# Kernel optimization log

Measured on AMD Instinct MI355X. Metric: run time of the kernel, lower is better.

## Reference

```python
import jax, jax.numpy as jnp
import numpy as np

N, E, F, H, C, K = 100000, 1600000, 512, 256, 64, 10
EPS = 1e-5  # BatchNorm1d default eps


def setup_inputs() -> dict:
    key = jax.random.key(0)
    ks = jax.random.split(key, 8)
    x = jax.random.normal(ks[0], (N, F), jnp.float32)
    # edge list with no self-loops (gcn_norm adds the self-loops itself)
    src = jax.random.randint(ks[1], (E,), 0, N)
    off = jax.random.randint(ks[2], (E,), 1, N)
    dst = (src + off) % N
    edge_index = jnp.stack([src, dst])
    s = lambda k, sh: jax.random.normal(k, sh, jnp.float32) * 0.02
    W0 = s(ks[3], (F, H)); b0 = jnp.zeros((H,), jnp.float32)
    g0 = jnp.ones((H,), jnp.float32); be0 = jnp.zeros((H,), jnp.float32)
    W1 = s(ks[4], (H, H)); b1 = jnp.zeros((H,), jnp.float32)
    g1 = jnp.ones((H,), jnp.float32); be1 = jnp.zeros((H,), jnp.float32)
    W2 = s(ks[5], (H, C)); b2 = jnp.zeros((C,), jnp.float32)
    proj_w = s(ks[6], (C, 1)); proj_b = jnp.zeros((1,), jnp.float32)
    return dict(x=x, W0=W0, b0=b0, g0=g0, be0=be0, W1=W1, b1=b1, g1=g1,
                be1=be1, W2=W2, b2=b2, proj_w=proj_w, proj_b=proj_b,
                edge_index=edge_index)


def _batchnorm(h, gamma, beta):
    # training-mode BN over the node (batch) axis, biased variance like torch
    mu = h.mean(0)
    var = h.var(0)
    return gamma * (h - mu) * jax.lax.rsqrt(var + EPS) + beta


def _prop(x, edge_index, proj_w, proj_b):
    n, c = x.shape
    loop = jnp.arange(n, dtype=edge_index.dtype)
    row = jnp.concatenate([edge_index[0], loop])  # message sources (x_j)
    col = jnp.concatenate([edge_index[1], loop])  # aggregation targets
    w = jnp.ones(row.shape, x.dtype)
    deg = jax.ops.segment_sum(w, col, num_segments=n)
    dis = jnp.where(deg > 0, jax.lax.rsqrt(jnp.maximum(deg, 1.0)) * (deg > 0), 0.0)
    dis = jnp.where(deg > 0, deg ** -0.5, 0.0)
    norm = dis[row] * dis[col]  # symmetric GCN normalization per edge

    def hop(xk, _):
        msgs = norm[:, None] * xk[row]               # gather + scale  [E+N, C]
        xk = jax.ops.segment_sum(msgs, col, num_segments=n)  # scatter-add
        return xk, xk

    _, hops = jax.lax.scan(hop, x, None, length=K)   # [K, N, C]
    pps = jnp.concatenate([x[None], hops], axis=0).transpose(1, 0, 2)  # [N, K+1, C]
    score = jax.nn.sigmoid(pps @ proj_w + proj_b)[..., 0]  # [N, K+1]
    return jnp.einsum('nk,nkc->nc', score, pps)      # [N, C]


def reference(x, W0, b0, g0, be0, W1, b1, g1, be1, W2, b2, proj_w, proj_b,
              edge_index):
    h = jax.nn.relu(_batchnorm(x @ W0 + b0, g0, be0))   # dropout is identity (eval)
    h = jax.nn.relu(_batchnorm(h @ W1 + b1, g1, be1))
    h = h @ W2 + b2                                     # [N, C] logits
    out = _prop(h, edge_index, proj_w, proj_b)
    return jax.nn.log_softmax(out, axis=1)
```

## Files before the change

### kernel.cpp

```cpp
#include <hip/hip_runtime.h>
#include <hip/hip_bf16.h>
#include <math.h>

#define NN 100000
#define FF 512
#define HH 256
#define CC 64
#define KHOPS 10
#define BN_EPS 1e-5f
#define NPART 8
#define DRANGE ((NN + NPART - 1) / NPART)

typedef __bf16 bf16x8 __attribute__((ext_vector_type(8)));
typedef float f32x4 __attribute__((ext_vector_type(4)));
typedef unsigned short ushort8v __attribute__((ext_vector_type(8)));

__device__ __forceinline__ unsigned short f2bf(float f) {
    __bf16 b = (__bf16)f;
    return __builtin_bit_cast(unsigned short, b);
}
__device__ __forceinline__ float bf2f(unsigned short h) {
    unsigned u = ((unsigned)h) << 16;
    return __builtin_bit_cast(float, u);
}
__device__ __forceinline__ float lo16(unsigned u) { return bf2f((unsigned short)(u & 0xFFFF)); }
__device__ __forceinline__ float hi16(unsigned u) { return bf2f((unsigned short)(u >> 16)); }
__device__ __forceinline__ unsigned pk(float a, float b) {
    return ((unsigned)f2bf(b) << 16) | (unsigned)f2bf(a);
}

typedef __attribute__((address_space(1))) const void g_void;
typedef __attribute__((address_space(3))) void l_void;
__device__ __forceinline__ void gl2lds16(const void* g, void* l) {
    __builtin_amdgcn_global_load_lds((g_void*)g, (l_void*)l, 16, 0, 0);
}

template <int N>
__device__ __forceinline__ void waitcnt_vm() {
    if constexpr (N == 0) asm volatile("s_waitcnt vmcnt(0)" ::: "memory");
    else if constexpr (N == 1) asm volatile("s_waitcnt vmcnt(1)" ::: "memory");
    else if constexpr (N == 2) asm volatile("s_waitcnt vmcnt(2)" ::: "memory");
    else if constexpr (N == 3) asm volatile("s_waitcnt vmcnt(3)" ::: "memory");
    else if constexpr (N == 4) asm volatile("s_waitcnt vmcnt(4)" ::: "memory");
    else if constexpr (N == 5) asm volatile("s_waitcnt vmcnt(5)" ::: "memory");
    else if constexpr (N == 6) asm volatile("s_waitcnt vmcnt(6)" ::: "memory");
    else asm volatile("s_waitcnt vmcnt(8)" ::: "memory");
}

__global__ void k_zero(float* p, int n) {
    int i = blockIdx.x * blockDim.x + threadIdx.x;
    if (i < n) p[i] = 0.f;
}

__global__ void k_deg_init(int* deg, int n) {
    int i = blockIdx.x * blockDim.x + threadIdx.x;
    if (i < n) deg[i] = 1;
}

__global__ __launch_bounds__(256) void k_deg_part(const int* __restrict__ dst, int e,
                                                  int* __restrict__ deg) {
    __shared__ int hist[DRANGE];
    int part = blockIdx.x & 7;
    int lo = part * DRANGE;
    int range = min(DRANGE, NN - lo);
    for (int i = threadIdx.x; i < range; i += blockDim.x) hist[i] = 0;
    __syncthreads();
    int nsub = gridDim.x >> 3, sub = blockIdx.x >> 3;
    for (int i = sub * blockDim.x + threadIdx.x; i < e; i += nsub * blockDim.x) {
        int d = dst[i] - lo;
        if ((unsigned)d < (unsigned)range) atomicAdd(&hist[d], 1);
    }
    __syncthreads();
    for (int i = threadIdx.x; i < range; i += blockDim.x) {
        int v = hist[i];
        if (v) atomicAdd(&deg[lo + i], v);
    }
}

__global__ void k_dis(const int* __restrict__ deg, float* dis, int n) {
    int i = blockIdx.x * blockDim.x + threadIdx.x;
    if (i < n) dis[i] = rsqrtf((float)deg[i]);
}

#define SCAN_B 1024
#define SCAN_NB ((NN + SCAN_B - 1) / SCAN_B)

__global__ void k_scan1(const int* __restrict__ deg, int* __restrict__ part, int n) {
    __shared__ int ls[SCAN_B];
    int i = blockIdx.x * SCAN_B + threadIdx.x;
    ls[threadIdx.x] = (i < n) ? deg[i] - 1 : 0;
    __syncthreads();
    for (int d = SCAN_B / 2; d > 0; d >>= 1) {
        if (threadIdx.x < d) ls[threadIdx.x] += ls[threadIdx.x + d];
        __syncthreads();
    }
    if (threadIdx.x == 0) part[blockIdx.x] = ls[0];
}

__global__ void k_scan2(int* part, int* offs_last, int nb) {
    if (threadIdx.x == 0) {
        int run = 0;
        for (int b = 0; b < nb; b++) { int v = part[b]; part[b] = run; run += v; }
        offs_last[0] = run;
    }
}

__global__ void k_scan3(const int* __restrict__ deg, const int* __restrict__ part,
                        int* __restrict__ offs, int* __restrict__ cur, int n) {
    __shared__ int ls[SCAN_B];
    int i = blockIdx.x * SCAN_B + threadIdx.x;
    int v = (i < n) ? deg[i] - 1 : 0;
    ls[threadIdx.x] = v;
    __syncthreads();
    for (int d = 1; d < SCAN_B; d <<= 1) {
        int t = (threadIdx.x >= d) ? ls[threadIdx.x - d] : 0;
        __syncthreads();
        ls[threadIdx.x] += t;
        __syncthreads();
    }
    if (i < n) {
        int ex = part[blockIdx.x] + ls[threadIdx.x] - v;
        offs[i] = ex;
        cur[i] = ex;
    }
}

__global__ __launch_bounds__(256) void k_fill_part(
    const int* __restrict__ src, const int* __restrict__ dst, int e,
    int* __restrict__ cursor, int* __restrict__ csrc) {
    int part = blockIdx.x & 7;
    int lo = part * DRANGE;
    int range = min(DRANGE, NN - lo);
    int nsub = gridDim.x >> 3, sub = blockIdx.x >> 3;
    for (int i = sub * blockDim.x + threadIdx.x; i < e; i += nsub * blockDim.x) {
        int d = dst[i];
        int dl = d - lo;
        if ((unsigned)dl < (unsigned)range) {
            int p = atomicAdd(&cursor[d], 1);
            csrc[p] = src[i];
        }
    }
}

__global__ void k_wt(const float* __restrict__ W, unsigned short* __restrict__ Wt,
                     int K, int N) {
    int i = blockIdx.x * blockDim.x + threadIdx.x;
    if (i < K * N) {
        int n = i / K;
        int k = i - n * K;
        Wt[i] = f2bf(W[(size_t)k * N + n]);
    }
}

template <int AF32, int BN_, int STATS, int NW, int FUSEBN, int ZSCALE>
__global__ __launch_bounds__(NW * 64) void k_gemm_mfma(
    const void* __restrict__ Av, const unsigned short* __restrict__ Bt,
    const float* __restrict__ bias, unsigned short* __restrict__ Cb,
    const float* __restrict__ bnscale, const float* __restrict__ bnshift,
    const float* __restrict__ disp,
    float* __restrict__ sum, float* __restrict__ sumsq,
    int M, int K, int Nd) {
    constexpr int NT = NW * 64;
    constexpr int WC = (NW == 8) ? 4 : 2;
    constexpr int PWN = BN_ / WC;
    constexpr int NREP = PWN / 16;
    constexpr int ACH = AF32 ? 8 : 4;
    constexpr int AOPS = 128 * ACH / NT;
    constexpr int BOPS = BN_ * 4 / NT;
    constexpr int S = AOPS + BOPS;
    constexpr int ABUF = AF32 ? 16384 : 8192;
    __shared__ __align__(16) unsigned char Asb[2][ABUF];
    __shared__ __align__(16) unsigned char Bsb[2][BN_ * 64];
    const int tid = threadIdx.x;
    const int lane = tid & 63;
    const int wid = tid >> 6;
    const int wrow = wid / WC, wcol = wid % WC;
    const int row_base = blockIdx.y * 128;
    const int col_base = blockIdx.x * BN_;
    const unsigned char* Abase = (const unsigned char*)Av;
    const size_t arowb = (size_t)K * (AF32 ? 4 : 2);

    f32x4 acc[4][NREP];
#pragma unroll
    for (int m = 0; m < 4; m++)
#pragma unroll
        for (int n = 0; n < NREP; n++)
#pragma unroll
            for (int j = 0; j < 4; j++) acc[m][n][j] = 0.f;

    auto stage = [&](int kt, int buf) {
#pragma unroll
        for (int i = 0; i < AOPS; ++i) {
            int e = i * NT + tid;
            int r = e / ACH;
            int c = e % ACH;
            int cs = AF32 ? (c ^ (r & 7)) : (c ^ ((r >> 1) & 3));
            int grow = row_base + r;
            if (grow > M - 1) grow = M - 1;
            const void* g = Abase + (size_t)grow * arowb + (size_t)kt * (AF32 ? 4 : 2) + (cs << 4);
            gl2lds16(g, Asb[buf] + e * 16);
        }
#pragma unroll
        for (int i = 0; i < BOPS; ++i) {
            int e = i * NT + tid;
            int r = e >> 2, c = e & 3;
            int cs = c ^ ((r >> 1) & 3);
            const void* g = (const unsigned char*)Bt + (size_t)(col_base + r) * (K * 2) +
                            (size_t)kt * 2 + (cs << 4);
            gl2lds16(g, Bsb[buf] + e * 16);
        }
    };

    const int nt = K / 32;
    stage(0, 0);
    if (nt > 1) stage(32, 1);

    for (int t = 0; t < nt; ++t) {
        if (t + 1 < nt) waitcnt_vm<S>();
        else            waitcnt_vm<0>();
        __builtin_amdgcn_s_barrier();
        const int cur = t & 1;

        f32x4 sc0{}, sc1{}, sh0{}, sh1{};
        if (FUSEBN) {
            int kc = t * 32 + (lane >> 4) * 8;
            sc0 = *(const f32x4*)(bnscale + kc);
            sc1 = *(const f32x4*)(bnscale + kc + 4);
            sh0 = *(const f32x4*)(bnshift + kc);
            sh1 = *(const f32x4*)(bnshift + kc + 4);
        }

        bf16x8 af[4], bfr[NREP];
#pragma unroll
        for (int m = 0; m < 4; ++m) {
            int r = wrow * 64 + m * 16 + (lane & 15);
            if (AF32) {
                int x7 = r & 7;
                int q2 = (lane >> 4) * 2;
                f32x4 f0 = *(const f32x4*)(Asb[cur] + r * 128 + ((q2 ^ x7) << 4));
                f32x4 f1 = *(const f32x4*)(Asb[cur] + r * 128 + (((q2 + 1) ^ x7) << 4));
                bf16x8 a;
                a[0] = (__bf16)f0[0]; a[1] = (__bf16)f0[1]; a[2] = (__bf16)f0[2]; a[3] = (__bf16)f0[3];
                a[4] = (__bf16)f1[0]; a[5] = (__bf16)f1[1]; a[6] = (__bf16)f1[2]; a[7] = (__bf16)f1[3];
                af[m] = a;
            } else {
                int cs = (lane >> 4) ^ ((r >> 1) & 3);
                bf16x8 a = *(const bf16x8*)(Asb[cur] + r * 64 + (cs << 4));
                if (FUSEBN) {
#pragma unroll
                    for (int j = 0; j < 4; ++j) {
                        a[j]     = (__bf16)fmaxf((float)a[j]     * sc0[j] + sh0[j], 0.f);
                        a[j + 4] = (__bf16)fmaxf((float)a[j + 4] * sc1[j] + sh1[j], 0.f);
                    }
                }
                af[m] = a;
            }
        }
#pragma unroll
        for (int n = 0; n < NREP; ++n) {
            int r = wcol * PWN + n * 16 + (lane & 15);
            int cs = (lane >> 4) ^ ((r >> 1) & 3);
            bfr[n] = *(const bf16x8*)(Bsb[cur] + r * 64 + (cs << 4));
        }
#pragma unroll
        for (int m = 0; m < 4; ++m)
#pragma unroll
            for (int n = 0; n < NREP; ++n)
                acc[m][n] = __builtin_amdgcn_mfma_f32_16x16x32_bf16(af[m], bfr[n], acc[m][n], 0, 0, 0);

        __builtin_amdgcn_s_barrier();
        if (t + 2 < nt) stage((t + 2) * 32, cur);
    }

    const int lc = lane & 15;
    const int lr = (lane >> 4) * 4;
#pragma unroll
    for (int m = 0; m < 4; ++m) {
        int gr0 = row_base + wrow * 64 + m * 16 + lr;
#pragma unroll
        for (int n = 0; n < NREP; ++n) {
            int gc = col_base + wcol * PWN + n * 16 + lc;
            float bb = bias[gc];
#pragma unroll
            for (int j = 0; j < 4; ++j) {
                int gr = gr0 + j;
                if (gr < M) {
                    float v = acc[m][n][j] + bb;
                    if (ZSCALE) v *= disp[gr];
                    Cb[(size_t)gr * Nd + gc] = f2bf(v);
                }
            }
        }
    }
    if (STATS) {
#pragma unroll
        for (int n = 0; n < NREP; ++n) {
            int gc = col_base + wcol * PWN + n * 16 + lc;
            float bb = bias[gc];
            float s = 0.f, s2 = 0.f;
#pragma unroll
            for (int m = 0; m < 4; ++m) {
                int gr0 = row_base + wrow * 64 + m * 16 + lr;
#pragma unroll
                for (int j = 0; j < 4; ++j) {
                    if (gr0 + j < M) {
                        float v = acc[m][n][j] + bb;
                        s += v;
                        s2 += v * v;
                    }
                }
            }
            s += __shfl_xor(s, 16); s += __shfl_xor(s, 32);
            s2 += __shfl_xor(s2, 16); s2 += __shfl_xor(s2, 32);
            if ((lane >> 4) == 0) {
                atomicAdd(&sum[gc], s);
                atomicAdd(&sumsq[gc], s2);
            }
        }
    }
}

__global__ void k_bnfin(const float* __restrict__ sum, const float* __restrict__ sq,
                        const float* __restrict__ g, const float* __restrict__ be,
                        float* scale, float* shift) {
    int c = threadIdx.x;
    float mu = sum[c] * (1.f / NN);
    float var = sq[c] * (1.f / NN) - mu * mu;
    float sc = g[c] * rsqrtf(var + BN_EPS);
    scale[c] = sc;
    shift[c] = be[c] - mu * sc;
}

__global__ void k_hop(const unsigned short* __restrict__ zin,
                      unsigned short* __restrict__ zout,
                      const int* __restrict__ offs, const int* __restrict__ csrc,
                      const float* __restrict__ dis, int n) {
    int wid = (int)((blockIdx.x * (size_t)blockDim.x + threadIdx.x) >> 6);
    if (wid >= n) return;
    int lane = threadIdx.x & 63;
    int g = lane >> 3;
    int j = lane & 7;
    const uint4* z16 = (const uint4*)zin;
    float y0 = 0.f, y1 = 0.f, y2 = 0.f, y3 = 0.f, y4 = 0.f, y5 = 0.f, y6 = 0.f, y7 = 0.f;
    if (g == 0) {
        uint4 v = z16[(size_t)wid * 8 + j];
        y0 = lo16(v.x); y1 = hi16(v.x);
        y2 = lo16(v.y); y3 = hi16(v.y);
        y4 = lo16(v.z); y5 = hi16(v.z);
        y6 = lo16(v.w); y7 = hi16(v.w);
    }
    int p0 = offs[wid], p1 = offs[wid + 1];
    int p = p0 + g;
    for (; p + 8 < p1; p += 16) {
        int sA = __builtin_nontemporal_load(&csrc[p]);
        int sB = __builtin_nontemporal_load(&csrc[p + 8]);
        uint4 vA = z16[(size_t)sA * 8 + j];
        uint4 vB = z16[(size_t)sB * 8 + j];
        y0 += lo16(vA.x); y1 += hi16(vA.x);
        y2 += lo16(vA.y); y3 += hi16(vA.y);
        y4 += lo16(vA.z); y5 += hi16(vA.z);
        y6 += lo16(vA.w); y7 += hi16(vA.w);
        y0 += lo16(vB.x); y1 += hi16(vB.x);
        y2 += lo16(vB.y); y3 += hi16(vB.y);
        y4 += lo16(vB.z); y5 += hi16(vB.z);
        y6 += lo16(vB.w); y7 += hi16(vB.w);
    }
    for (; p < p1; p += 8) {
        int s = __builtin_nontemporal_load(&csrc[p]);
        uint4 v = z16[(size_t)s * 8 + j];
        y0 += lo16(v.x); y1 += hi16(v.x);
        y2 += lo16(v.y); y3 += hi16(v.y);
        y4 += lo16(v.z); y5 += hi16(v.z);
        y6 += lo16(v.w); y7 += hi16(v.w);
    }
#pragma unroll
    for (int m = 8; m <= 32; m <<= 1) {
        y0 += __shfl_xor(y0, m); y1 += __shfl_xor(y1, m);
        y2 += __shfl_xor(y2, m); y3 += __shfl_xor(y3, m);
        y4 += __shfl_xor(y4, m); y5 += __shfl_xor(y5, m);
        y6 += __shfl_xor(y6, m); y7 += __shfl_xor(y7, m);
    }
    if (g == 0) {
        float dn = dis[wid];
        float d2 = dn * dn;
        uint4 r;
        r.x = pk(d2 * y0, d2 * y1); r.y = pk(d2 * y2, d2 * y3);
        r.z = pk(d2 * y4, d2 * y5); r.w = pk(d2 * y6, d2 * y7);
        ((uint4*)zout)[(size_t)wid * 8 + j] = r;
    }
}

struct XPack { const unsigned short* p[KHOPS + 1]; };

__global__ void k_finprop(XPack xp, const float* __restrict__ pw,
                          const float* __restrict__ pbp, const float* __restrict__ dis,
                          float* __restrict__ out, int n) {
    int gw = (int)((blockIdx.x * (size_t)blockDim.x + threadIdx.x) >> 6);
    int lane = threadIdx.x & 63;
    int hf = lane >> 5;
    int l = lane & 31;
    int node = gw * 2 + hf;
    if (node >= n) return;
    float pw0 = pw[2 * l], pw1 = pw[2 * l + 1];
    float pb0 = pbp[0];
    float invd = 1.f / dis[node];
    float o0 = 0.f, o1 = 0.f;
#pragma unroll
    for (int k = 0; k <= KHOPS; k++) {
        unsigned v = ((const unsigned*)xp.p[k])[(size_t)node * 32 + l];
        float v0 = lo16(v);
        float v1 = hi16(v);
        float d = v0 * pw0 + v1 * pw1;
#pragma unroll
        for (int m = 16; m >= 1; m >>= 1) d += __shfl_xor(d, m);
        float s = 1.f / (1.f + expf(-(d * invd + pb0)));
        o0 += s * v0;
        o1 += s * v1;
    }
    o0 *= invd;
    o1 *= invd;
    float mx = fmaxf(o0, o1);
#pragma unroll
    for (int m = 16; m >= 1; m >>= 1) mx = fmaxf(mx, __shfl_xor(mx, m));
    float e = expf(o0 - mx) + expf(o1 - mx);
#pragma unroll
    for (int m = 16; m >= 1; m >>= 1) e += __shfl_xor(e, m);
    float lg = mx + logf(e);
    float2 r = make_float2(o0 - lg, o1 - lg);
    *(float2*)(out + (size_t)node * 64 + 2 * l) = r;
}

extern "C" void kernel_launch(void* const* d_in, const int* in_sizes, int n_in,
                              void* d_out, int out_size, void* d_ws, size_t ws_size,
                              hipStream_t stream) {
    const float* x  = (const float*)d_in[0];
    const float* W0 = (const float*)d_in[1];
    const float* b0 = (const float*)d_in[2];
    const float* g0 = (const float*)d_in[3];
    const float* be0 = (const float*)d_in[4];
    const float* W1 = (const float*)d_in[5];
    const float* b1 = (const float*)d_in[6];
    const float* g1 = (const float*)d_in[7];
    const float* be1 = (const float*)d_in[8];
    const float* W2 = (const float*)d_in[9];
    const float* b2 = (const float*)d_in[10];
    const float* pw = (const float*)d_in[11];
    const float* pb = (const float*)d_in[12];
    const int* ei = (const int*)d_in[13];
    const int E = in_sizes[13] / 2;
    const int* esrc = ei;
    const int* edst = ei + E;

    char* ws = (char*)d_ws;
    const size_t XKB = (size_t)NN * CC * 2;
    unsigned short* h0b = (unsigned short*)(ws + 0);
    unsigned short* h1b = (unsigned short*)(ws + 51200000);
    unsigned short* xk[KHOPS + 1];
    xk[0] = (unsigned short*)(ws + 0);
    xk[5] = (unsigned short*)(ws + XKB);
    xk[6] = (unsigned short*)(ws + 2 * XKB);
    xk[7] = (unsigned short*)(ws + 3 * XKB);
    xk[1] = (unsigned short*)(ws + 51200000);
    xk[2] = (unsigned short*)(ws + 51200000 + XKB);
    xk[3] = (unsigned short*)(ws + 51200000 + 2 * XKB);
    xk[4] = (unsigned short*)(ws + 51200000 + 3 * XKB);
    xk[8] = (unsigned short*)(ws + 102400000);
    xk[9] = (unsigned short*)(ws + 115200000);
    xk[10] = (unsigned short*)(ws + 128000000);

    int*   deg  = (int*)  (ws + 140800000);
    float* dis  = (float*)(ws + 141200000);
    int*   offs = (int*)  (ws + 141600000);
    int*   cur  = (int*)  (ws + 142000064);
    int*   csrc = (int*)  (ws + 142400064);
    float* stats = (float*)(ws + 155200064);
    int*   part = (int*)  (ws + 155208256);
    unsigned short* W0t = (unsigned short*)(ws + 155209280);
    unsigned short* W1t = (unsigned short*)(ws + 155471424);
    unsigned short* W2t = (unsigned short*)(ws + 155602496);

    float* sum0 = stats,        *sq0 = stats + 256;
    float* sum1 = stats + 512,  *sq1 = stats + 768;
    float* scale0 = stats + 1024, *shift0 = stats + 1280;
    float* scale1 = stats + 1536, *shift1 = stats + 1792;

    float* out = (float*)d_out;

    const int TPB = 256;
    int ngrid = (NN + TPB - 1) / TPB;
    int wgrid = (NN * 64 + TPB - 1) / TPB;
    int wgrid2 = (((NN + 1) / 2) * 64 + TPB - 1) / TPB;
    int mtiles = (NN + 127) / 128;

    k_zero<<<2, 1024, 0, stream>>>(stats, 2048);
    k_deg_init<<<ngrid, TPB, 0, stream>>>(deg, NN);
    k_deg_part<<<128, TPB, 0, stream>>>(edst, E, deg);
    k_dis<<<ngrid, TPB, 0, stream>>>(deg, dis, NN);
    k_scan1<<<SCAN_NB, SCAN_B, 0, stream>>>(deg, part, NN);
    k_scan2<<<1, 64, 0, stream>>>(part, offs + NN, SCAN_NB);
    k_scan3<<<SCAN_NB, SCAN_B, 0, stream>>>(deg, part, offs, cur, NN);
    k_fill_part<<<256, TPB, 0, stream>>>(esrc, edst, E, cur, csrc);

    k_wt<<<(FF * HH + TPB - 1) / TPB, TPB, 0, stream>>>(W0, W0t, FF, HH);
    k_wt<<<(HH * HH + TPB - 1) / TPB, TPB, 0, stream>>>(W1, W1t, HH, HH);
    k_wt<<<(HH * CC + TPB - 1) / TPB, TPB, 0, stream>>>(W2, W2t, HH, CC);

    k_gemm_mfma<1, 256, 1, 8, 0, 0><<<dim3(1, mtiles), 512, 0, stream>>>(
        x, W0t, b0, h0b, nullptr, nullptr, nullptr, sum0, sq0, NN, FF, HH);
    k_bnfin<<<1, 256, 0, stream>>>(sum0, sq0, g0, be0, scale0, shift0);

    k_gemm_mfma<0, 256, 1, 8, 1, 0><<<dim3(1, mtiles), 512, 0, stream>>>(
        h0b, W1t, b1, h1b, scale0, shift0, nullptr, sum1, sq1, NN, HH, HH);
    k_bnfin<<<1, 256, 0, stream>>>(sum1, sq1, g1, be1, scale1, shift1);

    k_gemm_mfma<0, 64, 0, 4, 1, 1><<<dim3(1, mtiles), 256, 0, stream>>>(
        h1b, W2t, b2, xk[0], scale1, shift1, dis, nullptr, nullptr, NN, HH, CC);

    for (int k = 0; k < KHOPS; k++)
        k_hop<<<wgrid, TPB, 0, stream>>>(xk[k], xk[k + 1], offs, csrc, dis, NN);

    XPack xp;
    for (int k = 0; k <= KHOPS; k++) xp.p[k] = xk[k];
    k_finprop<<<wgrid2, TPB, 0, stream>>>(xp, pw, pb, dis, out, NN);
}
```

Baseline: 1.085 ms.

## Use global atomics for degree count, parallel scan2, larger grids for CSR build

The degree histogram drops its LDS staging and atomically increments global degree counts directly, with a much larger grid for both degree counting and CSR fill. The serial single-thread block-offset scan becomes a 128-thread parallel Hillis-Steele scan. Edge-index loads use nontemporal hints, and the src load is moved inside the partition check so only matching edges read it. The aim is to cut the preprocessing stages' serial latency and raise occupancy, at the cost of more global atomic contention and eight redundant passes over dst across the larger grid.

```diff
diff --git a/kernel.cpp b/kernel.cpp
--- a/kernel.cpp
+++ b/kernel.cpp
@@ -59,21 +59,13 @@
 
 __global__ __launch_bounds__(256) void k_deg_part(const int* __restrict__ dst, int e,
                                                   int* __restrict__ deg) {
-    __shared__ int hist[DRANGE];
     int part = blockIdx.x & 7;
     int lo = part * DRANGE;
-    int range = min(DRANGE, NN - lo);
-    for (int i = threadIdx.x; i < range; i += blockDim.x) hist[i] = 0;
-    __syncthreads();
+    int hi = min(lo + DRANGE, NN);
     int nsub = gridDim.x >> 3, sub = blockIdx.x >> 3;
     for (int i = sub * blockDim.x + threadIdx.x; i < e; i += nsub * blockDim.x) {
-        int d = dst[i] - lo;
-        if ((unsigned)d < (unsigned)range) atomicAdd(&hist[d], 1);
-    }
-    __syncthreads();
-    for (int i = threadIdx.x; i < range; i += blockDim.x) {
-        int v = hist[i];
-        if (v) atomicAdd(&deg[lo + i], v);
+        int d = __builtin_nontemporal_load(&dst[i]);
+        if (d >= lo && d < hi) atomicAdd(&deg[d], 1);
     }
 }
 
@@ -98,11 +90,19 @@
 }
 
 __global__ void k_scan2(int* part, int* offs_last, int nb) {
-    if (threadIdx.x == 0) {
-        int run = 0;
-        for (int b = 0; b < nb; b++) { int v = part[b]; part[b] = run; run += v; }
-        offs_last[0] = run;
-    }
+    __shared__ int ls[128];
+    int t = threadIdx.x;
+    int v = (t < nb) ? part[t] : 0;
+    ls[t] = v;
+    __syncthreads();
+    for (int d = 1; d < 128; d <<= 1) {
+        int u = (t >= d) ? ls[t - d] : 0;
+        __syncthreads();
+        ls[t] += u;
+        __syncthreads();
+    }
+    if (t < nb) part[t] = ls[t] - v;
+    if (t == nb - 1) offs_last[0] = ls[t];
 }
 
 __global__ void k_scan3(const int* __restrict__ deg, const int* __restrict__ part,
@@ -130,14 +130,14 @@
     int* __restrict__ cursor, int* __restrict__ csrc) {
     int part = blockIdx.x & 7;
     int lo = part * DRANGE;
-    int range = min(DRANGE, NN - lo);
+    int hi = min(lo + DRANGE, NN);
     int nsub = gridDim.x >> 3, sub = blockIdx.x >> 3;
     for (int i = sub * blockDim.x + threadIdx.x; i < e; i += nsub * blockDim.x) {
-        int d = dst[i];
-        int dl = d - lo;
-        if ((unsigned)dl < (unsigned)range) {
+        int d = __builtin_nontemporal_load(&dst[i]);
+        if (d >= lo && d < hi) {
+            int s = __builtin_nontemporal_load(&src[i]);
             int p = atomicAdd(&cursor[d], 1);
-            csrc[p] = src[i];
+            csrc[p] = s;
         }
     }
 }
@@ -494,12 +494,12 @@
 
     k_zero<<<2, 1024, 0, stream>>>(stats, 2048);
     k_deg_init<<<ngrid, TPB, 0, stream>>>(deg, NN);
-    k_deg_part<<<128, TPB, 0, stream>>>(edst, E, deg);
+    k_deg_part<<<2048, TPB, 0, stream>>>(edst, E, deg);
     k_dis<<<ngrid, TPB, 0, stream>>>(deg, dis, NN);
     k_scan1<<<SCAN_NB, SCAN_B, 0, stream>>>(deg, part, NN);
-    k_scan2<<<1, 64, 0, stream>>>(part, offs + NN, SCAN_NB);
+    k_scan2<<<1, 128, 0, stream>>>(part, offs + NN, SCAN_NB);
     k_scan3<<<SCAN_NB, SCAN_B, 0, stream>>>(deg, part, offs, cur, NN);
-    k_fill_part<<<256, TPB, 0, stream>>>(esrc, edst, E, cur, csrc);
+    k_fill_part<<<2048, TPB, 0, stream>>>(esrc, edst, E, cur, csrc);
 
     k_wt<<<(FF * HH + TPB - 1) / TPB, TPB, 0, stream>>>(W0, W0t, FF, HH);
     k_wt<<<(HH * HH + TPB - 1) / TPB, TPB, 0, stream>>>(W1, W1t, HH, HH);
```

Result: faster. 910.6 us (-16.1%).
